# Performance work log

Measured on AMD Instinct MI355X. Metric: run time of the kernel, lower is better.

## Reference

```python
import jax, jax.numpy as jnp
import numpy as np

B, DIM, H, W = 2, 128, 64, 64
DH, HEADS, K = 32, 4, 7  # dim_head, num_heads = dim // dim_head, kernel_size


def _ln(x, g, b):
    mu = jnp.mean(x, -1, keepdims=True)
    var = jnp.mean((x - mu) ** 2, -1, keepdims=True)
    return (x - mu) * jax.lax.rsqrt(var + 1e-5) * g + b


def _na2d(x, qkv_w, qkv_b, rpb, proj_w, proj_b):
    # NATTEN-style 2D neighborhood attention, dilation=1, edge-clamped windows.
    Bb, Hh, Ww, C = x.shape
    k = K
    qkv = (x @ qkv_w.T + qkv_b).reshape(Bb, Hh, Ww, 3, HEADS, DH).transpose(3, 0, 4, 1, 2, 5)
    q = qkv[0] * (DH ** -0.5)  # [B, heads, H, W, dh]
    kt, vt = qkv[1], qkv[2]
    def starts(n):
        return jnp.clip(jnp.arange(n) - k // 2, 0, n - k)
    nh = starts(Hh)[:, None] + jnp.arange(k)  # [H, k] absolute neighbor rows
    nw = starts(Ww)[:, None] + jnp.arange(k)  # [W, k] absolute neighbor cols
    ih = nh[:, None, :, None]  # [H,1,k,1]
    iw = nw[None, :, None, :]  # [1,W,1,k]
    Kw = kt[:, :, ih, iw, :]   # [B, heads, H, W, k, k, dh]
    Vw = vt[:, :, ih, iw, :]
    attn = jnp.einsum('bnhwd,bnhwijd->bnhwij', q, Kw)  # [B,heads,H,W,k,k]
    # relative positional bias, indices in [0, 2k-2]
    bih = (nh - jnp.arange(Hh)[:, None] + (k - 1))[:, None, :, None]
    biw = (nw - jnp.arange(Ww)[:, None] + (k - 1))[None, :, None, :]
    attn = attn + rpb[:, bih, biw][None]
    attn = jax.nn.softmax(attn.reshape(Bb, HEADS, Hh, Ww, k * k), -1).reshape(Bb, HEADS, Hh, Ww, k, k)
    out = jnp.einsum('bnhwij,bnhwijd->bnhwd', attn, Vw)
    out = out.transpose(0, 2, 3, 1, 4).reshape(Bb, Hh, Ww, C)
    return out @ proj_w.T + proj_b


def setup_inputs() -> dict:
    key = jax.random.key(0)
    ks = jax.random.split(key, 8)
    d = DIM
    w = lambda k_, sh: jax.random.normal(k_, sh, jnp.float32) * 0.02
    inp = {'x': jax.random.normal(ks[0], (B, DIM, H, W), jnp.float32)}
    inp.update(g1=jnp.ones(d), be1=jnp.zeros(d), g2=jnp.ones(d), be2=jnp.zeros(d),
               g3=jnp.ones(d), be3=jnp.zeros(d), g4=jnp.ones(d), be4=jnp.zeros(d))
    inp['qkv_w'] = w(ks[1], (3 * d, d)); inp['qkv_b'] = jnp.zeros(3 * d)
    inp['rpb'] = w(ks[2], (HEADS, 2 * K - 1, 2 * K - 1))
    inp['proj_w'] = w(ks[3], (d, d)); inp['proj_b'] = jnp.zeros(d)
    inp['w1'] = w(ks[4], (d, d)); inp['bl1'] = jnp.zeros(d)
    inp['w2'] = w(ks[5], (d, d)); inp['bl2'] = jnp.zeros(d)
    inp['w3'] = w(ks[6], (d, d)); inp['bl3'] = jnp.zeros(d)
    return inp


def reference(x, g1, be1, g2, be2, g3, be3, g4, be4, qkv_w, qkv_b, rpb, proj_w, proj_b, w1, bl1, w2, bl2, w3, bl3):
    x = x.transpose(0, 2, 3, 1)  # NCHW -> NHWC
    r = x
    y = _ln(x, g1, be1)
    y = _na2d(y, qkv_w, qkv_b, rpb, proj_w, proj_b)
    y = _ln(y, g2, be2)
    y = y @ w1.T + bl1
    x = y + r
    r = x
    y = _ln(x, g3, be3)
    y = y @ w2.T + bl2
    y = jax.nn.relu(y)
    y = _ln(y, g4, be4)
    y = y @ w3.T + bl3
    x = y + r
    return x.transpose(0, 3, 1, 2)  # NHWC -> NCHW
```

## Files before the change

kernel.cpp:

```cpp
#include <hip/hip_runtime.h>
#include <hip/hip_bf16.h>
#include <cstdint>

typedef short bf16x8 __attribute__((ext_vector_type(8)));
typedef float f32x4 __attribute__((ext_vector_type(4)));

#define NTOK 8192
#define QSCALE 0.17677669529663687f

__device__ inline float b2f(short s) {
  return __uint_as_float(((unsigned)(unsigned short)s) << 16);
}
__device__ inline short f2bs(float x) {
  __hip_bfloat16 b = __float2bfloat16(x);
  return *reinterpret_cast<short*>(&b);
}
__device__ inline bf16x8 ld8(const short* p) {
  short4 lo = *reinterpret_cast<const short4*>(p);
  short4 hi = *reinterpret_cast<const short4*>(p + 4);
  bf16x8 r;
  r[0] = lo.x; r[1] = lo.y; r[2] = lo.z; r[3] = lo.w;
  r[4] = hi.x; r[5] = hi.y; r[6] = hi.z; r[7] = hi.w;
  return r;
}
__device__ inline bf16x8 cvt8(float4 a, float4 c) {
  bf16x8 r;
  r[0] = f2bs(a.x); r[1] = f2bs(a.y); r[2] = f2bs(a.z); r[3] = f2bs(a.w);
  r[4] = f2bs(c.x); r[5] = f2bs(c.y); r[6] = f2bs(c.z); r[7] = f2bs(c.w);
  return r;
}

__global__ __launch_bounds__(512) void k_qkvcw(
    const float* __restrict__ x, const float* __restrict__ g,
    const float* __restrict__ be, const float* __restrict__ qkv_b,
    const float* __restrict__ qkv_w, const float* __restrict__ pw,
    const float* __restrict__ w1f, const float* __restrict__ w2f,
    const float* __restrict__ w3f, __hip_bfloat16* __restrict__ wb,
    __hip_bfloat16* __restrict__ qkvb) {
  __shared__ float xt[128][17];
  __shared__ __hip_bfloat16 at[16][136];
  __shared__ __align__(16) __hip_bfloat16 qt[16][392];
  int t = threadIdx.x;
  if (t < 128) {
    int ci = blockIdx.x * 128 + t;
    float cv;
    if (ci < 16384) cv = pw[ci];
    else if (ci < 32768) cv = w1f[ci - 16384];
    else if (ci < 49152) cv = w2f[ci - 32768];
    else cv = w3f[ci - 49152];
    wb[ci] = __float2bfloat16(cv);
  }
  int bid = blockIdx.x;
  int swz = (bid & 7) * 64 + (bid >> 3);
  int m0 = swz * 16;
  int b = m0 >> 12;
  int p0 = m0 & 4095;
  const float* xb = x + (size_t)b * 524288;
  int tw = t & 15, th = t >> 4;
#pragma unroll
  for (int i = 0; i < 4; ++i) {
    int c = i * 32 + th;
    xt[c][tw] = xb[c * 4096 + p0 + tw];
  }
  __syncthreads();
  int wid = t >> 6, lane = t & 63;
  float gg0 = g[lane], gg1 = g[lane + 64];
  float bb0 = be[lane], bb1 = be[lane + 64];
#pragma unroll
  for (int it = 0; it < 2; ++it) {
    int tt = wid * 2 + it;
    float v0 = xt[lane][tt], v1 = xt[lane + 64][tt];
    float s = v0 + v1, sq = v0 * v0 + v1 * v1;
#pragma unroll
    for (int off = 32; off; off >>= 1) {
      s += __shfl_xor(s, off);
      sq += __shfl_xor(sq, off);
    }
    float mu = s * (1.f / 128.f);
    float var = sq * (1.f / 128.f) - mu * mu;
    float rs = rsqrtf(var + 1e-5f);
    at[tt][lane] = __float2bfloat16((v0 - mu) * rs * gg0 + bb0);
    at[tt][lane + 64] = __float2bfloat16((v1 - mu) * rs * gg1 + bb1);
  }
  __syncthreads();
  int lr = lane & 15, kg = lane >> 4;
  bf16x8 af[4];
#pragma unroll
  for (int ks = 0; ks < 4; ++ks)
    af[ks] = *reinterpret_cast<const bf16x8*>(&at[lr][ks * 32 + kg * 8]);
  f32x4 acc[3];
#pragma unroll
  for (int nf = 0; nf < 3; ++nf) acc[nf] = f32x4{0, 0, 0, 0};
#pragma unroll
  for (int nf = 0; nf < 3; ++nf) {
    int o = wid * 48 + nf * 16 + lr;
    const float* wp = qkv_w + o * 128 + kg * 8;
#pragma unroll
    for (int ks = 0; ks < 4; ++ks) {
      float4 wa = *reinterpret_cast<const float4*>(wp + ks * 32);
      float4 wc = *reinterpret_cast<const float4*>(wp + ks * 32 + 4);
      acc[nf] = __builtin_amdgcn_mfma_f32_16x16x32_bf16(af[ks], cvt8(wa, wc),
                                                        acc[nf], 0, 0, 0);
    }
  }
#pragma unroll
  for (int nf = 0; nf < 3; ++nf) {
    int o = wid * 48 + nf * 16 + lr;
    float bv = qkv_b[o];
    float qs = (o < 128) ? QSCALE : 1.f;
#pragma unroll
    for (int rr = 0; rr < 4; ++rr)
      qt[kg * 4 + rr][o] = __float2bfloat16((acc[nf][rr] + bv) * qs);
  }
  __syncthreads();
  for (int i = t; i < 768; i += 512) {
    int row = i / 48, col = i - row * 48;
    *reinterpret_cast<uint4*>(qkvb + (size_t)(m0 + row) * 384 + col * 8) =
        *reinterpret_cast<const uint4*>(&qt[row][col * 8]);
  }
}

#define NB 98
#define VP 108
#define VPD 54
#define PP 132
#define VTSH 13824
__global__ __launch_bounds__(512, 4) void k_fuse3(
    const __hip_bfloat16* __restrict__ qkvb, const float* __restrict__ rpb,
    const float* __restrict__ x, const __hip_bfloat16* __restrict__ wb,
    const float* __restrict__ bproj,
    const float* __restrict__ g2, const float* __restrict__ be2,
    const float* __restrict__ b1,
    const float* __restrict__ g3, const float* __restrict__ be3,
    const float* __restrict__ b2,
    const float* __restrict__ g4, const float* __restrict__ be4,
    const float* __restrict__ b3, float* __restrict__ out) {
  __shared__ __align__(16) short smem[2 * VTSH + 2 * 4 * 8 * PP];
  __shared__ __align__(16) __hip_bfloat16 abuf[16][136];
  __shared__ float2 red[8][16];
  const short* qs = (const short*)qkvb;
  int tid = threadIdx.x;
  int bid = blockIdx.x;
  int swz = (bid & 7) * 64 + (bid >> 3);
  int m0 = swz * 16;
  int b = m0 >> 12, hq = (m0 >> 6) & 63;
  int hs = min(max(hq - 3, 0), 57);
  const __hip_bfloat16* wproj = wb;
  const __hip_bfloat16* w1 = wb + 16384;
  const __hip_bfloat16* w2 = wb + 32768;
  const __hip_bfloat16* w3 = wb + 49152;

  {
    int half = tid >> 8;
    int tl = tid & 255;
    int c0h = (m0 & 63) + half * 8;
    int csh = min(max(c0h - 3, 0), 50);
    unsigned* VtD = (unsigned*)(smem + half * VTSH);
    int g2i = tl >> 6, rp = tl & 63;
    if (rp < 49) {
      int r0 = rp * 2, r1 = r0 + 1;
      int rh0 = r0 / 14, rc0 = r0 - rh0 * 14;
      int rh1 = r1 / 14, rc1 = r1 - rh1 * 14;
      int tr0 = b * 4096 + (hs + rh0) * 64 + min(csh + rc0, 63);
      int tr1 = b * 4096 + (hs + rh1) * 64 + min(csh + rc1, 63);
#pragma unroll
      for (int gg = 0; gg < 4; ++gg) {
        int d0 = (g2i * 4 + gg) * 8;
        const short* p0 = qs + (size_t)tr0 * 384 + 256 + d0;
        const short* p1 = qs + (size_t)tr1 * 384 + 256 + d0;
        short4 a0 = *(const short4*)p0, a1 = *(const short4*)(p0 + 4);
        short4 c0v = *(const short4*)p1, c1 = *(const short4*)(p1 + 4);
        unsigned bse = (unsigned)d0 * VPD + rp;
        VtD[bse + 0 * VPD] = (unsigned short)a0.x | ((unsigned)(unsigned short)c0v.x << 16);
        VtD[bse + 1 * VPD] = (unsigned short)a0.y | ((unsigned)(unsigned short)c0v.y << 16);
        VtD[bse + 2 * VPD] = (unsigned short)a0.z | ((unsigned)(unsigned short)c0v.z << 16);
        VtD[bse + 3 * VPD] = (unsigned short)a0.w | ((unsigned)(unsigned short)c0v.w << 16);
        VtD[bse + 4 * VPD] = (unsigned short)a1.x | ((unsigned)(unsigned short)c1.x << 16);
        VtD[bse + 5 * VPD] = (unsigned short)a1.y | ((unsigned)(unsigned short)c1.y << 16);
        VtD[bse + 6 * VPD] = (unsigned short)a1.z | ((unsigned)(unsigned short)c1.z << 16);
        VtD[bse + 7 * VPD] = (unsigned short)a1.w | ((unsigned)(unsigned short)c1.w << 16);
      }
    }
    for (int i = tl; i < 128 * 5; i += 256) {
      int d = i / 5, j = i - d * 5;
      VtD[d * VPD + 49 + j] = 0;
    }
  }

  int wid = tid >> 6, lane = tid & 63;
  int sst = wid >> 2, h = wid & 3;
  int lr = lane & 15, kg = lane >> 4;
  int m0s = m0 + sst * 8;
  int c0s = (m0 & 63) + sst * 8;
  int cs0 = min(max(c0s - 3, 0), 50);
  int qrow = min(m0s + lr, NTOK - 1);
  bf16x8 aq = *reinterpret_cast<const bf16x8*>(qs + (size_t)qrow * 384 + h * 32 + kg * 8);
  f32x4 sc[7];
#pragma unroll
  for (int nt = 0; nt < 7; ++nt) {
    int nbr = nt * 16 + lr;
    int rw = min(nbr, NB - 1);
    int rh = rw / 14, rc = rw - rh * 14;
    int tn = b * 4096 + (hs + rh) * 64 + min(cs0 + rc, 63);
    bf16x8 bk = *reinterpret_cast<const bf16x8*>(qs + (size_t)tn * 384 + 128 + h * 32 + kg * 8);
    sc[nt] = __builtin_amdgcn_mfma_f32_16x16x32_bf16(aq, bk, f32x4{0, 0, 0, 0}, 0, 0, 0);
  }
  int offv[4], cmt[4];
#pragma unroll
  for (int rr = 0; rr < 4; ++rr) {
    int ct = c0s + kg * 4 + rr;
    int ws0 = min(max(ct - 3, 0), 57);
    offv[rr] = ws0 - cs0;
    cmt[rr] = cs0 + 6 - ct;
  }
  float mx[4] = {-3e38f, -3e38f, -3e38f, -3e38f};
#pragma unroll
  for (int nt = 0; nt < 7; ++nt) {
    int nbr = nt * 16 + lr;
    int rh = nbr / 14, rc = nbr - rh * 14;
    bool vn = nbr < NB;
    int ribase = h * 169 + (hs - hq + 6 + rh) * 13 + rc;
#pragma unroll
    for (int rr = 0; rr < 4; ++rr) {
      float v = -1e30f;
      if (vn && (unsigned)(rc - offv[rr]) < 7u) v = sc[nt][rr] + rpb[ribase + cmt[rr]];
      sc[nt][rr] = v;
      mx[rr] = fmaxf(mx[rr], v);
    }
  }
#pragma unroll
  for (int rr = 0; rr < 4; ++rr) {
    mx[rr] = fmaxf(mx[rr], __shfl_xor(mx[rr], 1));
    mx[rr] = fmaxf(mx[rr], __shfl_xor(mx[rr], 2));
    mx[rr] = fmaxf(mx[rr], __shfl_xor(mx[rr], 4));
    mx[rr] = fmaxf(mx[rr], __shfl_xor(mx[rr], 8));
  }
  float sum[4] = {0.f, 0.f, 0.f, 0.f};
#pragma unroll
  for (int nt = 0; nt < 7; ++nt)
#pragma unroll
    for (int rr = 0; rr < 4; ++rr) {
      float e = __expf(sc[nt][rr] - mx[rr]);
      sc[nt][rr] = e;
      sum[rr] += e;
    }
#pragma unroll
  for (int rr = 0; rr < 4; ++rr) {
    sum[rr] += __shfl_xor(sum[rr], 1);
    sum[rr] += __shfl_xor(sum[rr], 2);
    sum[rr] += __shfl_xor(sum[rr], 4);
    sum[rr] += __shfl_xor(sum[rr], 8);
  }
  short* Ph = smem + 2 * VTSH + ((sst * 4 + h) * 8) * PP;
  if (kg < 2) {
#pragma unroll
    for (int rr = 0; rr < 4; ++rr) {
      float inv = 1.f / sum[rr];
      int tok = kg * 4 + rr;
#pragma unroll
      for (int nt = 0; nt < 7; ++nt)
        Ph[tok * PP + nt * 16 + lr] = f2bs(sc[nt][rr] * inv);
      Ph[tok * PP + 112 + lr] = 0;
      Ph[tok * PP + 128 + (lr & 3)] = 0;
    }
  }
  __syncthreads();
  {
    const short* Vts = smem + sst * VTSH;
    f32x4 o2[2] = {f32x4{0, 0, 0, 0}, f32x4{0, 0, 0, 0}};
#pragma unroll
    for (int kt = 0; kt < 4; ++kt) {
      bf16x8 ap = ld8(Ph + (lr & 7) * PP + kt * 32 + kg * 8);
#pragma unroll
      for (int dt = 0; dt < 2; ++dt) {
        bf16x8 bv = ld8(Vts + (h * 32 + dt * 16 + lr) * VP + kt * 32 + kg * 8);
        o2[dt] = __builtin_amdgcn_mfma_f32_16x16x32_bf16(ap, bv, o2[dt], 0, 0, 0);
      }
    }
    if (kg < 2) {
#pragma unroll
      for (int dt = 0; dt < 2; ++dt)
#pragma unroll
        for (int rr = 0; rr < 4; ++rr)
          abuf[sst * 8 + kg * 4 + rr][h * 32 + dt * 16 + lr] =
              __float2bfloat16(o2[dt][rr]);
    }
  }
  __syncthreads();

  f32x4 acc;
  float x2f[4];

  auto gemm_lds = [&](const __hip_bfloat16* W) {
    bf16x8 af[4];
#pragma unroll
    for (int ks = 0; ks < 4; ++ks)
      af[ks] = *reinterpret_cast<const bf16x8*>(&abuf[lr][ks * 32 + kg * 8]);
    int o = wid * 16 + lr;
    const __hip_bfloat16* wp = W + o * 128 + kg * 8;
    acc = f32x4{0, 0, 0, 0};
#pragma unroll
    for (int ks = 0; ks < 4; ++ks) {
      bf16x8 bfr = *reinterpret_cast<const bf16x8*>(wp + ks * 32);
      acc = __builtin_amdgcn_mfma_f32_16x16x32_bf16(af[ks], bfr, acc, 0, 0, 0);
    }
  };
  auto ln_store = [&](const float* g, const float* be) {
    float ps[4], pq[4];
#pragma unroll
    for (int rr = 0; rr < 4; ++rr) {
      ps[rr] = acc[rr];
      pq[rr] = acc[rr] * acc[rr];
    }
#pragma unroll
    for (int rr = 0; rr < 4; ++rr)
#pragma unroll
      for (int off = 1; off < 16; off <<= 1) {
        ps[rr] += __shfl_xor(ps[rr], off);
        pq[rr] += __shfl_xor(pq[rr], off);
      }
    if (lr == 0)
#pragma unroll
      for (int rr = 0; rr < 4; ++rr)
        red[wid][kg * 4 + rr] = make_float2(ps[rr], pq[rr]);
    __syncthreads();
    float mu[4], rs[4];
#pragma unroll
    for (int rr = 0; rr < 4; ++rr) {
      int r16 = kg * 4 + rr;
      float ssum = 0.f, qsum = 0.f;
#pragma unroll
      for (int w = 0; w < 8; ++w) {
        float2 a = red[w][r16];
        ssum += a.x;
        qsum += a.y;
      }
      mu[rr] = ssum * (1.f / 128.f);
      float var = qsum * (1.f / 128.f) - mu[rr] * mu[rr];
      rs[rr] = rsqrtf(var + 1e-5f);
    }
    int o = wid * 16 + lr;
    float gv = g[o], bev = be[o];
#pragma unroll
    for (int rr = 0; rr < 4; ++rr)
      abuf[kg * 4 + rr][o] =
          __float2bfloat16((acc[rr] - mu[rr]) * rs[rr] * gv + bev);
    __syncthreads();
  };

  gemm_lds(wproj);
  {
    float bv = bproj[wid * 16 + lr];
#pragma unroll
    for (int rr = 0; rr < 4; ++rr) acc[rr] += bv;
  }
  ln_store(g2, be2);

  gemm_lds(w1);
  {
    int o = wid * 16 + lr;
    float bv = b1[o];
#pragma unroll
    for (int rr = 0; rr < 4; ++rr) {
      int m = m0 + kg * 4 + rr;
      float v = acc[rr] + bv +
                x[(size_t)(m >> 12) * 524288 + (size_t)o * 4096 + (m & 4095)];
      x2f[rr] = v;
      acc[rr] = v;
    }
  }
  ln_store(g3, be3);

  gemm_lds(w2);
  {
    float bv = b2[wid * 16 + lr];
#pragma unroll
    for (int rr = 0; rr < 4; ++rr) acc[rr] = fmaxf(acc[rr] + bv, 0.f);
  }
  ln_store(g4, be4);

  gemm_lds(w3);
  {
    int o = wid * 16 + lr;
    float bv = b3[o];
#pragma unroll
    for (int rr = 0; rr < 4; ++rr) {
      int m = m0 + kg * 4 + rr;
      float v = acc[rr] + bv + x2f[rr];
      int bb = m >> 12, hw = m & 4095;
      out[(size_t)bb * 524288 + o * 4096 + hw] = v;
    }
  }
}

extern "C" void kernel_launch(void* const* d_in, const int* in_sizes, int n_in,
                              void* d_out, int out_size, void* d_ws,
                              size_t ws_size, hipStream_t stream) {
  const float* x = (const float*)d_in[0];
  const float* g1 = (const float*)d_in[1];
  const float* be1 = (const float*)d_in[2];
  const float* g2 = (const float*)d_in[3];
  const float* be2 = (const float*)d_in[4];
  const float* g3 = (const float*)d_in[5];
  const float* be3 = (const float*)d_in[6];
  const float* g4 = (const float*)d_in[7];
  const float* be4 = (const float*)d_in[8];
  const float* qkv_w = (const float*)d_in[9];
  const float* qkv_b = (const float*)d_in[10];
  const float* rpb = (const float*)d_in[11];
  const float* proj_w = (const float*)d_in[12];
  const float* proj_b = (const float*)d_in[13];
  const float* w1 = (const float*)d_in[14];
  const float* bl1 = (const float*)d_in[15];
  const float* w2 = (const float*)d_in[16];
  const float* bl2 = (const float*)d_in[17];
  const float* w3 = (const float*)d_in[18];
  const float* bl3 = (const float*)d_in[19];

  char* ws = (char*)d_ws;
  __hip_bfloat16* wb = (__hip_bfloat16*)ws;
  __hip_bfloat16* qkvb = (__hip_bfloat16*)(ws + 4456448);

  k_qkvcw<<<512, 512, 0, stream>>>(x, g1, be1, qkv_b, qkv_w, proj_w, w1, w2,
                                   w3, wb, qkvb);
  k_fuse3<<<512, 512, 0, stream>>>(qkvb, rpb, x, wb, proj_b, g2, be2, bl1, g3,
                                   be3, bl2, g4, be4, bl3, (float*)d_out);
}
```

Baseline: 45.74 us.

## Fuse QKV and attention kernels into one persistent kernel with flag-based sync

Merges the LN1+QKV projection kernel and the attention/MLP kernel into a single launch. Each block writes its QKV tile, then publishes a per-tile ready flag and bumps a global counter. Before attention it spins on the flags of the neighboring row tiles it needs, and before the projection GEMMs it waits for every block to finish converting the weights. This removes one kernel launch and the full device-wide barrier between the stages, but adds a memset, spin-waits, and a deadlock risk if all 512 blocks cannot be resident at the same time.

```diff
diff --git a/kernel.cpp b/kernel.cpp
--- a/kernel.cpp
+++ b/kernel.cpp
@@ -30,121 +30,134 @@
   return r;
 }
 
-__global__ __launch_bounds__(512) void k_qkvcw(
-    const float* __restrict__ x, const float* __restrict__ g,
-    const float* __restrict__ be, const float* __restrict__ qkv_b,
-    const float* __restrict__ qkv_w, const float* __restrict__ pw,
-    const float* __restrict__ w1f, const float* __restrict__ w2f,
-    const float* __restrict__ w3f, __hip_bfloat16* __restrict__ wb,
-    __hip_bfloat16* __restrict__ qkvb) {
-  __shared__ float xt[128][17];
-  __shared__ __hip_bfloat16 at[16][136];
-  __shared__ __align__(16) __hip_bfloat16 qt[16][392];
-  int t = threadIdx.x;
-  if (t < 128) {
-    int ci = blockIdx.x * 128 + t;
-    float cv;
-    if (ci < 16384) cv = pw[ci];
-    else if (ci < 32768) cv = w1f[ci - 16384];
-    else if (ci < 49152) cv = w2f[ci - 32768];
-    else cv = w3f[ci - 49152];
-    wb[ci] = __float2bfloat16(cv);
-  }
-  int bid = blockIdx.x;
-  int swz = (bid & 7) * 64 + (bid >> 3);
-  int m0 = swz * 16;
-  int b = m0 >> 12;
-  int p0 = m0 & 4095;
-  const float* xb = x + (size_t)b * 524288;
-  int tw = t & 15, th = t >> 4;
-#pragma unroll
-  for (int i = 0; i < 4; ++i) {
-    int c = i * 32 + th;
-    xt[c][tw] = xb[c * 4096 + p0 + tw];
-  }
-  __syncthreads();
-  int wid = t >> 6, lane = t & 63;
-  float gg0 = g[lane], gg1 = g[lane + 64];
-  float bb0 = be[lane], bb1 = be[lane + 64];
-#pragma unroll
-  for (int it = 0; it < 2; ++it) {
-    int tt = wid * 2 + it;
-    float v0 = xt[lane][tt], v1 = xt[lane + 64][tt];
-    float s = v0 + v1, sq = v0 * v0 + v1 * v1;
-#pragma unroll
-    for (int off = 32; off; off >>= 1) {
-      s += __shfl_xor(s, off);
-      sq += __shfl_xor(sq, off);
-    }
-    float mu = s * (1.f / 128.f);
-    float var = sq * (1.f / 128.f) - mu * mu;
-    float rs = rsqrtf(var + 1e-5f);
-    at[tt][lane] = __float2bfloat16((v0 - mu) * rs * gg0 + bb0);
-    at[tt][lane + 64] = __float2bfloat16((v1 - mu) * rs * gg1 + bb1);
-  }
-  __syncthreads();
-  int lr = lane & 15, kg = lane >> 4;
-  bf16x8 af[4];
-#pragma unroll
-  for (int ks = 0; ks < 4; ++ks)
-    af[ks] = *reinterpret_cast<const bf16x8*>(&at[lr][ks * 32 + kg * 8]);
-  f32x4 acc[3];
-#pragma unroll
-  for (int nf = 0; nf < 3; ++nf) acc[nf] = f32x4{0, 0, 0, 0};
-#pragma unroll
-  for (int nf = 0; nf < 3; ++nf) {
-    int o = wid * 48 + nf * 16 + lr;
-    const float* wp = qkv_w + o * 128 + kg * 8;
-#pragma unroll
-    for (int ks = 0; ks < 4; ++ks) {
-      float4 wa = *reinterpret_cast<const float4*>(wp + ks * 32);
-      float4 wc = *reinterpret_cast<const float4*>(wp + ks * 32 + 4);
-      acc[nf] = __builtin_amdgcn_mfma_f32_16x16x32_bf16(af[ks], cvt8(wa, wc),
-                                                        acc[nf], 0, 0, 0);
-    }
-  }
-#pragma unroll
-  for (int nf = 0; nf < 3; ++nf) {
-    int o = wid * 48 + nf * 16 + lr;
-    float bv = qkv_b[o];
-    float qs = (o < 128) ? QSCALE : 1.f;
-#pragma unroll
-    for (int rr = 0; rr < 4; ++rr)
-      qt[kg * 4 + rr][o] = __float2bfloat16((acc[nf][rr] + bv) * qs);
-  }
-  __syncthreads();
-  for (int i = t; i < 768; i += 512) {
-    int row = i / 48, col = i - row * 48;
-    *reinterpret_cast<uint4*>(qkvb + (size_t)(m0 + row) * 384 + col * 8) =
-        *reinterpret_cast<const uint4*>(&qt[row][col * 8]);
-  }
-}
-
 #define NB 98
 #define VP 108
 #define VPD 54
 #define PP 132
 #define VTSH 13824
-__global__ __launch_bounds__(512, 4) void k_fuse3(
-    const __hip_bfloat16* __restrict__ qkvb, const float* __restrict__ rpb,
-    const float* __restrict__ x, const __hip_bfloat16* __restrict__ wb,
+__global__ __launch_bounds__(512, 4) void k_mega(
+    const float* __restrict__ x, const float* __restrict__ g1,
+    const float* __restrict__ be1, const float* __restrict__ qkv_b,
+    const float* __restrict__ qkv_w, const float* __restrict__ pw,
+    const float* __restrict__ w1f, const float* __restrict__ w2f,
+    const float* __restrict__ w3f, __hip_bfloat16* __restrict__ wb,
+    __hip_bfloat16* __restrict__ qkvb, const float* __restrict__ rpb,
     const float* __restrict__ bproj,
     const float* __restrict__ g2, const float* __restrict__ be2,
     const float* __restrict__ b1,
     const float* __restrict__ g3, const float* __restrict__ be3,
     const float* __restrict__ b2,
     const float* __restrict__ g4, const float* __restrict__ be4,
-    const float* __restrict__ b3, float* __restrict__ out) {
+    const float* __restrict__ b3, float* __restrict__ out,
+    int* __restrict__ flags, int* __restrict__ cnt) {
   __shared__ __align__(16) short smem[2 * VTSH + 2 * 4 * 8 * PP];
   __shared__ __align__(16) __hip_bfloat16 abuf[16][136];
   __shared__ float2 red[8][16];
-  const short* qs = (const short*)qkvb;
-  int tid = threadIdx.x;
+  int t = threadIdx.x;
   int bid = blockIdx.x;
   int swz = (bid & 7) * 64 + (bid >> 3);
   int m0 = swz * 16;
   int b = m0 >> 12, hq = (m0 >> 6) & 63;
   int hs = min(max(hq - 3, 0), 57);
+
+  {
+    char* lbase = (char*)smem;
+    float(*xt)[17] = reinterpret_cast<float(*)[17]>(lbase);
+    __hip_bfloat16(*at)[136] =
+        reinterpret_cast<__hip_bfloat16(*)[136]>(lbase + 8704);
+    __hip_bfloat16(*qt)[392] =
+        reinterpret_cast<__hip_bfloat16(*)[392]>(lbase + 8704 + 4352);
+    if (t < 128) {
+      int ci = bid * 128 + t;
+      float cv;
+      if (ci < 16384) cv = pw[ci];
+      else if (ci < 32768) cv = w1f[ci - 16384];
+      else if (ci < 49152) cv = w2f[ci - 32768];
+      else cv = w3f[ci - 49152];
+      wb[ci] = __float2bfloat16(cv);
+    }
+    int p0 = m0 & 4095;
+    const float* xb = x + (size_t)b * 524288;
+    int tw = t & 15, th = t >> 4;
+#pragma unroll
+    for (int i = 0; i < 4; ++i) {
+      int c = i * 32 + th;
+      xt[c][tw] = xb[c * 4096 + p0 + tw];
+    }
+    __syncthreads();
+    int wid = t >> 6, lane = t & 63;
+    float gg0 = g1[lane], gg1v = g1[lane + 64];
+    float bb0 = be1[lane], bb1 = be1[lane + 64];
+#pragma unroll
+    for (int it = 0; it < 2; ++it) {
+      int tt = wid * 2 + it;
+      float v0 = xt[lane][tt], v1 = xt[lane + 64][tt];
+      float s = v0 + v1, sq = v0 * v0 + v1 * v1;
+#pragma unroll
+      for (int off = 32; off; off >>= 1) {
+        s += __shfl_xor(s, off);
+        sq += __shfl_xor(sq, off);
+      }
+      float mu = s * (1.f / 128.f);
+      float var = sq * (1.f / 128.f) - mu * mu;
+      float rs = rsqrtf(var + 1e-5f);
+      at[tt][lane] = __float2bfloat16((v0 - mu) * rs * gg0 + bb0);
+      at[tt][lane + 64] = __float2bfloat16((v1 - mu) * rs * gg1v + bb1);
+    }
+    __syncthreads();
+    int lr = lane & 15, kg = lane >> 4;
+    bf16x8 af[4];
+#pragma unroll
+    for (int ks = 0; ks < 4; ++ks)
+      af[ks] = *reinterpret_cast<const bf16x8*>(&at[lr][ks * 32 + kg * 8]);
+    f32x4 acc[3];
+#pragma unroll
+    for (int nf = 0; nf < 3; ++nf) acc[nf] = f32x4{0, 0, 0, 0};
+#pragma unroll
+    for (int nf = 0; nf < 3; ++nf) {
+      int o = wid * 48 + nf * 16 + lr;
+      const float* wp = qkv_w + o * 128 + kg * 8;
+#pragma unroll
+      for (int ks = 0; ks < 4; ++ks) {
+        float4 wa = *reinterpret_cast<const float4*>(wp + ks * 32);
+        float4 wc = *reinterpret_cast<const float4*>(wp + ks * 32 + 4);
+        acc[nf] = __builtin_amdgcn_mfma_f32_16x16x32_bf16(af[ks], cvt8(wa, wc),
+                                                          acc[nf], 0, 0, 0);
+      }
+    }
+#pragma unroll
+    for (int nf = 0; nf < 3; ++nf) {
+      int o = wid * 48 + nf * 16 + lr;
+      float bv = qkv_b[o];
+      float qsc = (o < 128) ? QSCALE : 1.f;
+#pragma unroll
+      for (int rr = 0; rr < 4; ++rr)
+        qt[kg * 4 + rr][o] = __float2bfloat16((acc[nf][rr] + bv) * qsc);
+    }
+    __syncthreads();
+    for (int i = t; i < 768; i += 512) {
+      int row = i / 48, col = i - row * 48;
+      *reinterpret_cast<uint4*>(qkvb + (size_t)(m0 + row) * 384 + col * 8) =
+          *reinterpret_cast<const uint4*>(&qt[row][col * 8]);
+    }
+  }
+  __threadfence();
+  __syncthreads();
+  if (t == 0) {
+    __hip_atomic_store(&flags[swz], 1, __ATOMIC_RELEASE, __HIP_MEMORY_SCOPE_AGENT);
+    __hip_atomic_fetch_add(cnt, 1, __ATOMIC_RELEASE, __HIP_MEMORY_SCOPE_AGENT);
+  }
+
+  {
+    int f0 = b * 256 + hs * 4;
+    if (t < 28)
+      while (__hip_atomic_load(&flags[f0 + t], __ATOMIC_ACQUIRE,
+                               __HIP_MEMORY_SCOPE_AGENT) == 0) {}
+    __syncthreads();
+  }
+
+  const short* qs = (const short*)qkvb;
+  int tid = t;
   const __hip_bfloat16* wproj = wb;
   const __hip_bfloat16* w1 = wb + 16384;
   const __hip_bfloat16* w2 = wb + 32768;
@@ -286,6 +299,10 @@
               __float2bfloat16(o2[dt][rr]);
     }
   }
+  __syncthreads();
+
+  if (t == 0)
+    while (__hip_atomic_load(cnt, __ATOMIC_ACQUIRE, __HIP_MEMORY_SCOPE_AGENT) < 512) {}
   __syncthreads();
 
   f32x4 acc;
@@ -419,10 +436,12 @@
 
   char* ws = (char*)d_ws;
   __hip_bfloat16* wb = (__hip_bfloat16*)ws;
+  int* flags = (int*)(ws + 262144);
+  int* cnt = flags + 512;
   __hip_bfloat16* qkvb = (__hip_bfloat16*)(ws + 4456448);
 
-  k_qkvcw<<<512, 512, 0, stream>>>(x, g1, be1, qkv_b, qkv_w, proj_w, w1, w2,
-                                   w3, wb, qkvb);
-  k_fuse3<<<512, 512, 0, stream>>>(qkvb, rpb, x, wb, proj_b, g2, be2, bl1, g3,
-                                   be3, bl2, g4, be4, bl3, (float*)d_out);
-}
+  hipMemsetAsync(flags, 0, 513 * sizeof(int), stream);
+  k_mega<<<512, 512, 0, stream>>>(x, g1, be1, qkv_b, qkv_w, proj_w, w1, w2, w3,
+                                  wb, qkvb, rpb, proj_b, g2, be2, bl1, g3, be3,
+                                  bl2, g4, be4, bl3, (float*)d_out, flags, cnt);
+}
```

Result: slower. 161.1 us (+252.2%).
